# Kernel tuning notes

Hardware: AMD Instinct MI355X
Metric: run time of the kernel (lower is better)

The kernel has to match this reference:

```python
import jax, jax.numpy as jnp
import numpy as np

# Static conv / spline hyperparameters (match init_kwargs)
KH = KW = 3
SH = SW = 1          # stride
DH = DW = 1          # dilation
GRID_SIZE = 5
SPLINE_ORDER = 3
N_CONVS = 8


def _extract_patches(x):
    """im2col unfold. x: (B,C,H,W) -> (B,C,Ho,Wo,KH*KW), valid padding."""
    B, C, H, W = x.shape
    Ho = (H - (KH - 1) * DH - 1) // SH + 1
    Wo = (W - (KW - 1) * DW - 1) // SW + 1
    cols = []
    for i in range(KH):
        for j in range(KW):
            cols.append(x[:, :,
                          i * DH: i * DH + (Ho - 1) * SH + 1: SH,
                          j * DW: j * DW + (Wo - 1) * SW + 1: SW])
    return jnp.stack(cols, axis=-1), Ho, Wo


def _b_splines(xf, grid):
    """Cox-de Boor recursion. xf: (P,K), grid: (K, G+2*so+1) -> (P,K,G+so)."""
    x = xf[:, :, None]
    bases = ((x >= grid[:, :-1]) & (x < grid[:, 1:])).astype(xf.dtype)
    for k in range(1, SPLINE_ORDER + 1):
        bases = ((x - grid[:, :-(k + 1)]) / (grid[:, k:-1] - grid[:, :-(k + 1)])
                 * bases[:, :, :-1]
                 + (grid[:, k + 1:] - x) / (grid[:, k + 1:] - grid[:, 1:-k])
                 * bases[:, :, 1:])
    return bases


def setup_inputs() -> dict:
    key = jax.random.key(0)
    k0, k1, k2, k3 = jax.random.split(key, 4)
    B, C, H, W = 8, 32, 64, 64
    K = KH * KW                       # in_features of KANLinear = 9
    coeff = GRID_SIZE + SPLINE_ORDER  # spline coefficients per input = 8
    # activations inside grid_range [-1, 1]
    x = jax.random.uniform(k0, (B, C, H, W), jnp.float32, -1.0, 1.0)
    # grid buffer: arange(-so, gs+so+1)*h + grid_range[0], tiled per input feature
    h = (1.0 - (-1.0)) / GRID_SIZE
    g = jnp.arange(-SPLINE_ORDER, GRID_SIZE + SPLINE_ORDER + 1,
                   dtype=jnp.float32) * h - 1.0
    grid = jnp.tile(g[None, :], (K, 1))  # (K, 12)
    base_weight = jax.random.normal(k1, (N_CONVS, K), jnp.float32) / np.sqrt(K)
    spline_weight = jax.random.normal(k2, (N_CONVS, K, coeff), jnp.float32) * 0.1
    spline_scaler = jax.random.normal(k3, (N_CONVS, K), jnp.float32) / np.sqrt(K) + 1.0
    return {"x": x, "grid": grid, "base_weight": base_weight,
            "spline_weight": spline_weight, "spline_scaler": spline_scaler}


def reference(x, grid, base_weight, spline_weight, spline_scaler):
    B, C, H, W = x.shape
    patches, Ho, Wo = _extract_patches(x)          # (B,C,Ho,Wo,K)
    K = KH * KW
    xf = patches.reshape(-1, K)                    # (P, K), P = B*C*Ho*Wo
    # KANLinear: base path (SiLU + linear) + spline path (B-spline basis + linear)
    base_out = jnp.einsum('pk,vk->pv', jax.nn.silu(xf), base_weight)
    bases = _b_splines(xf, grid)                   # (P, K, coeff)
    scaled_sw = spline_weight * spline_scaler[:, :, None]
    spline_out = jnp.einsum('pkc,vkc->pv', bases, scaled_sw)
    out = (base_out + spline_out).reshape(B, C, Ho, Wo, N_CONVS)
    # channel-major then conv ordering: out[:, kern + channel*n_convs]
    return out.transpose(0, 1, 4, 2, 3).reshape(B, C * N_CONVS, Ho, Wo)
```

## Files before the change

kernel.cpp:

```cpp
#include <hip/hip_runtime.h>

typedef _Float16 f16;
typedef _Float16 f16x8 __attribute__((ext_vector_type(8)));
typedef float    f32x4 __attribute__((ext_vector_type(4)));

#define HO 62
#define WO 62

__global__ __launch_bounds__(384) void kan_prep(
    const float* __restrict__ bw, const float* __restrict__ sw,
    const float* __restrict__ sc, f16x8* __restrict__ ws)
{
    const int tid  = threadIdx.x;
    const int lane = tid & 63;
    const int q    = tid >> 6;
    const int ki   = q >> 1;
    const int kjp  = q & 1;
    const int nn   = lane & 15;
    const int kb   = lane >> 4;
    f16x8 bf;
    #pragma unroll
    for (int e = 0; e < 8; ++e) {
        const int k    = kb * 8 + e;
        const int kj   = kjp * 2 + (k >> 4);
        const int slot = k & 15;
        float wv = 0.0f;
        if (nn < 8 && kj < 3 && slot < 9) {
            const int kk = ki * 3 + kj;
            wv = (slot == 0) ? bw[nn * 9 + kk]
                             : sw[(nn * 9 + kk) * 8 + (slot - 1)] * sc[nn * 9 + kk];
        }
        bf[e] = (f16)wv;
    }
    ws[q * 64 + lane] = bf;
}

#define SLICE 2896
__global__ __launch_bounds__(256, 4) void kan_main(
    const float* __restrict__ x,
    const float* __restrict__ grid_,
    const f16x8* __restrict__ ws,
    float* __restrict__ out)
{
    __shared__ __align__(16) f16 feat[4 * SLICE];

    const int tid  = threadIdx.x;
    const int lane = tid & 63;
    const int w    = tid >> 6;
    f16* wfeat = &feat[w * SLICE];

    const int unit  = blockIdx.x * 4 + w;
    const int plane = unit >> 5;
    const int chunk = (unit >> 2) & 7;
    const int s     = unit & 3;
    const int r0    = chunk * 8;
    const int c0    = s * 16;

    f16x8 bfrag[3][2];
    #pragma unroll
    for (int q = 0; q < 6; ++q)
        bfrag[q >> 1][q & 1] = ws[q * 64 + lane];

    if (lane < 2)
        *(f16x8*)&wfeat[2880 + lane * 8] = (f16x8){(f16)0.f,(f16)0.f,(f16)0.f,(f16)0.f,
                                                   (f16)0.f,(f16)0.f,(f16)0.f,(f16)0.f};

    const float g0    = grid_[0];
    const float inv_h = 1.0f / (grid_[1] - grid_[0]);
    const float* xp   = x + (size_t)plane * 4096;

    #pragma unroll
    for (int it = 0; it < 3; ++it) {
        const int p = it * 64 + lane;
        if (p < 180) {
            const int row = p / 18;
            const int col = p - row * 18;
            int gy = r0 + row; gy = (gy < 64) ? gy : 63;
            int gx = c0 + col; gx = (gx < 64) ? gx : 63;
            const float xv = xp[gy * 64 + gx];

            const float si = xv / (1.0f + __expf(-xv));
            const float u  = (xv - g0) * inv_h;
            int j = (int)floorf(u);
            j = (j < 3) ? 3 : ((j > 7) ? 7 : j);
            const float t   = u - (float)j;
            const float omt = 1.0f - t;
            const float t2  = t * t;
            const float t3  = t2 * t;
            const float c6  = 1.0f / 6.0f;
            const float bv0 = omt * omt * omt * c6;
            const float bv1 = (3.0f * t3 - 6.0f * t2 + 4.0f) * c6;
            const float bv2 = (-3.0f * t3 + 3.0f * t2 + 3.0f * t + 1.0f) * c6;
            const float bv3 = t3 * c6;

            f16* fp = &wfeat[p * 16];
            f16x8 z0 = {(f16)si, (f16)0.f, (f16)0.f, (f16)0.f,
                        (f16)0.f, (f16)0.f, (f16)0.f, (f16)0.f};
            f16x8 z1 = {(f16)0.f, (f16)0.f, (f16)0.f, (f16)0.f,
                        (f16)0.f, (f16)0.f, (f16)0.f, (f16)0.f};
            *(f16x8*)fp       = z0;
            *(f16x8*)(fp + 8) = z1;
            fp[j - 2] = (f16)bv0;
            fp[j - 1] = (f16)bv1;
            fp[j]     = (f16)bv2;
            fp[j + 1] = (f16)bv3;
        }
    }

    const int mI    = lane & 15;
    const int kb    = lane >> 4;
    const int nn    = mI;
    const int khalf = kb & 1;
    const int cAdd  = kb >> 1;
    const int aBase = (mI + cAdd) * 16 + khalf * 8;

    f16x8 af[3][2];
    #pragma unroll
    for (int kjp = 0; kjp < 2; ++kjp) {
        af[0][kjp] = *(const f16x8*)&wfeat[aBase + kjp * 32 + 0 * 288];
        af[1][kjp] = *(const f16x8*)&wfeat[aBase + kjp * 32 + 1 * 288];
    }

    #pragma unroll
    for (int i = 0; i < 8; ++i) {
        #pragma unroll
        for (int kjp = 0; kjp < 2; ++kjp)
            af[(i + 2) % 3][kjp] =
                *(const f16x8*)&wfeat[aBase + kjp * 32 + (i + 2) * 288];

        f32x4 acc = {0.f, 0.f, 0.f, 0.f};
        #pragma unroll
        for (int ki = 0; ki < 3; ++ki)
            #pragma unroll
            for (int kjp = 0; kjp < 2; ++kjp)
                acc = __builtin_amdgcn_mfma_f32_16x16x32_f16(
                          af[(i + ki) % 3][kjp], bfrag[ki][kjp], acc, 0, 0, 0);

        const int ho = r0 + i;
        if (nn < 8 && ho < HO) {
            const int cb = c0 + kb * 4;
            float* po = out + ((size_t)(plane * 8 + nn) * (HO * WO)) + ho * WO + cb;
            if (cb + 3 < WO) {
                float2 lo = {acc[0], acc[1]};
                float2 hi = {acc[2], acc[3]};
                *(float2*)po       = lo;
                *(float2*)(po + 2) = hi;
            } else {
                #pragma unroll
                for (int q = 0; q < 4; ++q)
                    if (cb + q < WO) po[q] = acc[q];
            }
        }
    }
}

extern "C" void kernel_launch(void* const* d_in, const int* in_sizes, int n_in,
                              void* d_out, int out_size, void* d_ws, size_t ws_size,
                              hipStream_t stream) {
    const float* x    = (const float*)d_in[0];
    const float* grid = (const float*)d_in[1];
    const float* bw   = (const float*)d_in[2];
    const float* sw   = (const float*)d_in[3];
    const float* sc   = (const float*)d_in[4];
    float* out = (float*)d_out;
    f16x8* ws  = (f16x8*)d_ws;

    kan_prep<<<1, 384, 0, stream>>>(bw, sw, sc, ws);
    kan_main<<<2048, 256, 0, stream>>>(x, grid, ws, out);
}
```

Measured before the change: 79.52 us.

## Process two column strips per wave with prefetched loads and padded LDS records

Each wave now handles two 16-column strips in sequence, and the grid is halved to 1024 blocks. The global loads for the second strip are issued before the MFMA loop of the first strip so their latency is hidden. The per-pixel LDS feature record grows from 16 to 24 halves, which changes the stride pattern to reduce bank conflicts on fragment reads. In exchange each block does more serial work and uses more LDS, which may lower parallelism and occupancy.

Result: slower. 81.33 us (+2.3%).

```diff
diff --git a/kernel.cpp b/kernel.cpp
--- a/kernel.cpp
+++ b/kernel.cpp
@@ -6,6 +6,10 @@
 
 #define HO 62
 #define WO 62
+
+#define RECSZ  24
+#define ROWST  (18 * RECSZ)
+#define SLICE  (10 * ROWST + RECSZ)
 
 __global__ __launch_bounds__(384) void kan_prep(
     const float* __restrict__ bw, const float* __restrict__ sw,
@@ -35,7 +39,6 @@
     ws[q * 64 + lane] = bf;
 }
 
-#define SLICE 2896
 __global__ __launch_bounds__(256, 4) void kan_main(
     const float* __restrict__ x,
     const float* __restrict__ grid_,
@@ -50,60 +53,42 @@
     f16* wfeat = &feat[w * SLICE];
 
     const int unit  = blockIdx.x * 4 + w;
-    const int plane = unit >> 5;
-    const int chunk = (unit >> 2) & 7;
-    const int s     = unit & 3;
+    const int plane = unit >> 4;
+    const int chunk = (unit >> 1) & 7;
+    const int sh    = unit & 1;
     const int r0    = chunk * 8;
-    const int c0    = s * 16;
 
     f16x8 bfrag[3][2];
     #pragma unroll
     for (int q = 0; q < 6; ++q)
         bfrag[q >> 1][q & 1] = ws[q * 64 + lane];
 
-    if (lane < 2)
-        *(f16x8*)&wfeat[2880 + lane * 8] = (f16x8){(f16)0.f,(f16)0.f,(f16)0.f,(f16)0.f,
-                                                   (f16)0.f,(f16)0.f,(f16)0.f,(f16)0.f};
+    {
+        f16x8 z = {(f16)0.f,(f16)0.f,(f16)0.f,(f16)0.f,
+                   (f16)0.f,(f16)0.f,(f16)0.f,(f16)0.f};
+        if (lane < 3) *(f16x8*)&wfeat[10 * ROWST + lane * 8] = z;
+    }
 
     const float g0    = grid_[0];
     const float inv_h = 1.0f / (grid_[1] - grid_[0]);
     const float* xp   = x + (size_t)plane * 4096;
 
+    int prow[3], pcol[3];
     #pragma unroll
     for (int it = 0; it < 3; ++it) {
         const int p = it * 64 + lane;
-        if (p < 180) {
-            const int row = p / 18;
-            const int col = p - row * 18;
-            int gy = r0 + row; gy = (gy < 64) ? gy : 63;
-            int gx = c0 + col; gx = (gx < 64) ? gx : 63;
-            const float xv = xp[gy * 64 + gx];
-
-            const float si = xv / (1.0f + __expf(-xv));
-            const float u  = (xv - g0) * inv_h;
-            int j = (int)floorf(u);
-            j = (j < 3) ? 3 : ((j > 7) ? 7 : j);
-            const float t   = u - (float)j;
-            const float omt = 1.0f - t;
-            const float t2  = t * t;
-            const float t3  = t2 * t;
-            const float c6  = 1.0f / 6.0f;
-            const float bv0 = omt * omt * omt * c6;
-            const float bv1 = (3.0f * t3 - 6.0f * t2 + 4.0f) * c6;
-            const float bv2 = (-3.0f * t3 + 3.0f * t2 + 3.0f * t + 1.0f) * c6;
-            const float bv3 = t3 * c6;
-
-            f16* fp = &wfeat[p * 16];
-            f16x8 z0 = {(f16)si, (f16)0.f, (f16)0.f, (f16)0.f,
-                        (f16)0.f, (f16)0.f, (f16)0.f, (f16)0.f};
-            f16x8 z1 = {(f16)0.f, (f16)0.f, (f16)0.f, (f16)0.f,
-                        (f16)0.f, (f16)0.f, (f16)0.f, (f16)0.f};
-            *(f16x8*)fp       = z0;
-            *(f16x8*)(fp + 8) = z1;
-            fp[j - 2] = (f16)bv0;
-            fp[j - 1] = (f16)bv1;
-            fp[j]     = (f16)bv2;
-            fp[j + 1] = (f16)bv3;
+        prow[it] = p / 18;
+        pcol[it] = p - prow[it] * 18;
+    }
+
+    float xv[3];
+    {
+        const int c0 = (2 * sh) * 16;
+        #pragma unroll
+        for (int it = 0; it < 3; ++it) {
+            int gy = r0 + prow[it]; gy = (gy < 64) ? gy : 63;
+            int gx = c0 + pcol[it]; gx = (gx < 64) ? gx : 63;
+            xv[it] = xp[gy * 64 + gx];
         }
     }
 
@@ -112,43 +97,91 @@
     const int nn    = mI;
     const int khalf = kb & 1;
     const int cAdd  = kb >> 1;
-    const int aBase = (mI + cAdd) * 16 + khalf * 8;
-
-    f16x8 af[3][2];
-    #pragma unroll
-    for (int kjp = 0; kjp < 2; ++kjp) {
-        af[0][kjp] = *(const f16x8*)&wfeat[aBase + kjp * 32 + 0 * 288];
-        af[1][kjp] = *(const f16x8*)&wfeat[aBase + kjp * 32 + 1 * 288];
-    }
-
-    #pragma unroll
-    for (int i = 0; i < 8; ++i) {
-        #pragma unroll
-        for (int kjp = 0; kjp < 2; ++kjp)
-            af[(i + 2) % 3][kjp] =
-                *(const f16x8*)&wfeat[aBase + kjp * 32 + (i + 2) * 288];
-
-        f32x4 acc = {0.f, 0.f, 0.f, 0.f};
-        #pragma unroll
-        for (int ki = 0; ki < 3; ++ki)
+    const int aBase = (mI + cAdd) * RECSZ + khalf * 8;
+
+    #pragma unroll
+    for (int t = 0; t < 2; ++t) {
+        const int c0 = (2 * sh + t) * 16;
+
+        #pragma unroll
+        for (int it = 0; it < 3; ++it) {
+            const int p = it * 64 + lane;
+            if (p < 180) {
+                const float xvv = xv[it];
+                const float si = xvv / (1.0f + __expf(-xvv));
+                const float u  = (xvv - g0) * inv_h;
+                int j = (int)floorf(u);
+                j = (j < 3) ? 3 : ((j > 7) ? 7 : j);
+                const float tt  = u - (float)j;
+                const float omt = 1.0f - tt;
+                const float t2  = tt * tt;
+                const float t3  = t2 * tt;
+                const float c6  = 1.0f / 6.0f;
+                const float bv0 = omt * omt * omt * c6;
+                const float bv1 = (3.0f * t3 - 6.0f * t2 + 4.0f) * c6;
+                const float bv2 = (-3.0f * t3 + 3.0f * t2 + 3.0f * tt + 1.0f) * c6;
+                const float bv3 = t3 * c6;
+
+                f16* fp = &wfeat[p * RECSZ];
+                f16x8 z0 = {(f16)si, (f16)0.f, (f16)0.f, (f16)0.f,
+                            (f16)0.f, (f16)0.f, (f16)0.f, (f16)0.f};
+                f16x8 z1 = {(f16)0.f, (f16)0.f, (f16)0.f, (f16)0.f,
+                            (f16)0.f, (f16)0.f, (f16)0.f, (f16)0.f};
+                *(f16x8*)fp       = z0;
+                *(f16x8*)(fp + 8) = z1;
+                fp[j - 2] = (f16)bv0;
+                fp[j - 1] = (f16)bv1;
+                fp[j]     = (f16)bv2;
+                fp[j + 1] = (f16)bv3;
+            }
+        }
+
+        if (t == 0) {
+            const int c1 = (2 * sh + 1) * 16;
+            #pragma unroll
+            for (int it = 0; it < 3; ++it) {
+                int gy = r0 + prow[it]; gy = (gy < 64) ? gy : 63;
+                int gx = c1 + pcol[it]; gx = (gx < 64) ? gx : 63;
+                xv[it] = xp[gy * 64 + gx];
+            }
+        }
+
+        f16x8 af[3][2];
+        #pragma unroll
+        for (int kjp = 0; kjp < 2; ++kjp) {
+            af[0][kjp] = *(const f16x8*)&wfeat[aBase + kjp * (2 * RECSZ) + 0 * ROWST];
+            af[1][kjp] = *(const f16x8*)&wfeat[aBase + kjp * (2 * RECSZ) + 1 * ROWST];
+        }
+
+        #pragma unroll
+        for (int i = 0; i < 8; ++i) {
             #pragma unroll
             for (int kjp = 0; kjp < 2; ++kjp)
-                acc = __builtin_amdgcn_mfma_f32_16x16x32_f16(
-                          af[(i + ki) % 3][kjp], bfrag[ki][kjp], acc, 0, 0, 0);
-
-        const int ho = r0 + i;
-        if (nn < 8 && ho < HO) {
-            const int cb = c0 + kb * 4;
-            float* po = out + ((size_t)(plane * 8 + nn) * (HO * WO)) + ho * WO + cb;
-            if (cb + 3 < WO) {
-                float2 lo = {acc[0], acc[1]};
-                float2 hi = {acc[2], acc[3]};
-                *(float2*)po       = lo;
-                *(float2*)(po + 2) = hi;
-            } else {
+                af[(i + 2) % 3][kjp] =
+                    *(const f16x8*)&wfeat[aBase + kjp * (2 * RECSZ) + (i + 2) * ROWST];
+
+            f32x4 acc = {0.f, 0.f, 0.f, 0.f};
+            #pragma unroll
+            for (int ki = 0; ki < 3; ++ki)
                 #pragma unroll
-                for (int q = 0; q < 4; ++q)
-                    if (cb + q < WO) po[q] = acc[q];
+                for (int kjp = 0; kjp < 2; ++kjp)
+                    acc = __builtin_amdgcn_mfma_f32_16x16x32_f16(
+                              af[(i + ki) % 3][kjp], bfrag[ki][kjp], acc, 0, 0, 0);
+
+            const int ho = r0 + i;
+            if (nn < 8 && ho < HO) {
+                const int cb = c0 + kb * 4;
+                float* po = out + ((size_t)(plane * 8 + nn) * (HO * WO)) + ho * WO + cb;
+                if (cb + 3 < WO) {
+                    float2 lo = {acc[0], acc[1]};
+                    float2 hi = {acc[2], acc[3]};
+                    *(float2*)po       = lo;
+                    *(float2*)(po + 2) = hi;
+                } else {
+                    #pragma unroll
+                    for (int q = 0; q < 4; ++q)
+                        if (cb + q < WO) po[q] = acc[q];
+                }
             }
         }
     }
@@ -166,5 +199,5 @@
     f16x8* ws  = (f16x8*)d_ws;
 
     kan_prep<<<1, 384, 0, stream>>>(bw, sw, sc, ws);
-    kan_main<<<2048, 256, 0, stream>>>(x, grid, ws, out);
+    kan_main<<<1024, 256, 0, stream>>>(x, grid, ws, out);
 }
```

## Fuse weight-prep kernel into main kernel and build spline rows in registers

Applied to the files above, without the earlier changes.

Removes the separate single-block weight preparation launch: each block of the main kernel now builds the f16 MFMA B fragments itself into shared memory and synchronizes before use. This drops one kernel launch and the global workspace round trip, at the cost of redundant weight prep (small global reads, some arithmetic, a barrier) in every one of the 2048 blocks. The basis-feature write also changes from zero-fill plus four scattered f16 stores at dynamic offsets to two full vector stores built with selects in registers.

Measured after the change: 82.16 us. 3.3% more time.

```diff
diff --git a/kernel.cpp b/kernel.cpp
--- a/kernel.cpp
+++ b/kernel.cpp
@@ -6,48 +6,57 @@
 
 #define HO 62
 #define WO 62
+#define SLICE 2896
 
-__global__ __launch_bounds__(384) void kan_prep(
-    const float* __restrict__ bw, const float* __restrict__ sw,
-    const float* __restrict__ sc, f16x8* __restrict__ ws)
-{
-    const int tid  = threadIdx.x;
-    const int lane = tid & 63;
-    const int q    = tid >> 6;
-    const int ki   = q >> 1;
-    const int kjp  = q & 1;
-    const int nn   = lane & 15;
-    const int kb   = lane >> 4;
-    f16x8 bf;
-    #pragma unroll
-    for (int e = 0; e < 8; ++e) {
-        const int k    = kb * 8 + e;
-        const int kj   = kjp * 2 + (k >> 4);
-        const int slot = k & 15;
-        float wv = 0.0f;
-        if (nn < 8 && kj < 3 && slot < 9) {
-            const int kk = ki * 3 + kj;
-            wv = (slot == 0) ? bw[nn * 9 + kk]
-                             : sw[(nn * 9 + kk) * 8 + (slot - 1)] * sc[nn * 9 + kk];
-        }
-        bf[e] = (f16)wv;
-    }
-    ws[q * 64 + lane] = bf;
-}
-
-#define SLICE 2896
-__global__ __launch_bounds__(256, 4) void kan_main(
+__global__ __launch_bounds__(256, 4) void kan_fused(
     const float* __restrict__ x,
     const float* __restrict__ grid_,
-    const f16x8* __restrict__ ws,
+    const float* __restrict__ bw,
+    const float* __restrict__ sw,
+    const float* __restrict__ sc,
     float* __restrict__ out)
 {
-    __shared__ __align__(16) f16 feat[4 * SLICE];
+    __shared__ __align__(16) f16x8 wsl[6 * 64];
+    __shared__ __align__(16) f16   feat[4 * SLICE];
 
     const int tid  = threadIdx.x;
     const int lane = tid & 63;
     const int w    = tid >> 6;
     f16* wfeat = &feat[w * SLICE];
+
+    for (int t = tid; t < 384; t += 256) {
+        const int l   = t & 63;
+        const int q   = t >> 6;
+        const int ki  = q >> 1;
+        const int kjp = q & 1;
+        const int nn  = l & 15;
+        const int kb  = l >> 4;
+        f16x8 bf;
+        #pragma unroll
+        for (int e = 0; e < 8; ++e) {
+            const int k    = kb * 8 + e;
+            const int kj   = kjp * 2 + (k >> 4);
+            const int slot = k & 15;
+            float wv = 0.0f;
+            if (nn < 8 && kj < 3 && slot < 9) {
+                const int kk = ki * 3 + kj;
+                wv = (slot == 0) ? bw[nn * 9 + kk]
+                                 : sw[(nn * 9 + kk) * 8 + (slot - 1)] * sc[nn * 9 + kk];
+            }
+            bf[e] = (f16)wv;
+        }
+        wsl[q * 64 + l] = bf;
+    }
+    __syncthreads();
+
+    f16x8 bfrag[3][2];
+    #pragma unroll
+    for (int q = 0; q < 6; ++q)
+        bfrag[q >> 1][q & 1] = wsl[q * 64 + lane];
+
+    if (lane < 2)
+        *(f16x8*)&wfeat[2880 + lane * 8] = (f16x8){(f16)0.f,(f16)0.f,(f16)0.f,(f16)0.f,
+                                                   (f16)0.f,(f16)0.f,(f16)0.f,(f16)0.f};
 
     const int unit  = blockIdx.x * 4 + w;
     const int plane = unit >> 5;
@@ -55,15 +64,6 @@
     const int s     = unit & 3;
     const int r0    = chunk * 8;
     const int c0    = s * 16;
-
-    f16x8 bfrag[3][2];
-    #pragma unroll
-    for (int q = 0; q < 6; ++q)
-        bfrag[q >> 1][q & 1] = ws[q * 64 + lane];
-
-    if (lane < 2)
-        *(f16x8*)&wfeat[2880 + lane * 8] = (f16x8){(f16)0.f,(f16)0.f,(f16)0.f,(f16)0.f,
-                                                   (f16)0.f,(f16)0.f,(f16)0.f,(f16)0.f};
 
     const float g0    = grid_[0];
     const float inv_h = 1.0f / (grid_[1] - grid_[0]);
@@ -83,27 +83,37 @@
             const float u  = (xv - g0) * inv_h;
             int j = (int)floorf(u);
             j = (j < 3) ? 3 : ((j > 7) ? 7 : j);
-            const float t   = u - (float)j;
-            const float omt = 1.0f - t;
-            const float t2  = t * t;
-            const float t3  = t2 * t;
+            const float tt  = u - (float)j;
+            const float omt = 1.0f - tt;
+            const float t2  = tt * tt;
+            const float t3  = t2 * tt;
             const float c6  = 1.0f / 6.0f;
             const float bv0 = omt * omt * omt * c6;
             const float bv1 = (3.0f * t3 - 6.0f * t2 + 4.0f) * c6;
-            const float bv2 = (-3.0f * t3 + 3.0f * t2 + 3.0f * t + 1.0f) * c6;
+            const float bv2 = (-3.0f * t3 + 3.0f * t2 + 3.0f * tt + 1.0f) * c6;
             const float bv3 = t3 * c6;
 
+            f16x8 r0v, r1v;
+            r0v[0] = (f16)si;
+            #pragma unroll
+            for (int f = 1; f < 8; ++f) {
+                float val = 0.0f;
+                val = (f == j - 2) ? bv0 : val;
+                val = (f == j - 1) ? bv1 : val;
+                val = (f == j)     ? bv2 : val;
+                val = (f == j + 1) ? bv3 : val;
+                r0v[f] = (f16)val;
+            }
+            {
+                float val = (8 == j + 1) ? bv3 : 0.0f;
+                r1v[0] = (f16)val;
+            }
+            #pragma unroll
+            for (int f = 1; f < 8; ++f) r1v[f] = (f16)0.f;
+
             f16* fp = &wfeat[p * 16];
-            f16x8 z0 = {(f16)si, (f16)0.f, (f16)0.f, (f16)0.f,
-                        (f16)0.f, (f16)0.f, (f16)0.f, (f16)0.f};
-            f16x8 z1 = {(f16)0.f, (f16)0.f, (f16)0.f, (f16)0.f,
-                        (f16)0.f, (f16)0.f, (f16)0.f, (f16)0.f};
-            *(f16x8*)fp       = z0;
-            *(f16x8*)(fp + 8) = z1;
-            fp[j - 2] = (f16)bv0;
-            fp[j - 1] = (f16)bv1;
-            fp[j]     = (f16)bv2;
-            fp[j + 1] = (f16)bv3;
+            *(f16x8*)fp       = r0v;
+            *(f16x8*)(fp + 8) = r1v;
         }
     }
 
@@ -163,8 +173,6 @@
     const float* sw   = (const float*)d_in[3];
     const float* sc   = (const float*)d_in[4];
     float* out = (float*)d_out;
-    f16x8* ws  = (f16x8*)d_ws;
 
-    kan_prep<<<1, 384, 0, stream>>>(bw, sw, sc, ws);
-    kan_main<<<2048, 256, 0, stream>>>(x, grid, ws, out);
+    kan_fused<<<2048, 256, 0, stream>>>(x, grid, bw, sw, sc, out);
 }
```
